# Kernel optimization log

Measured on AMD Instinct MI355X. Metric: run time of the kernel, lower is better.

## Reference

```python
import jax, jax.numpy as jnp
import numpy as np

N_QUBITS = 14
STATE_DIM = 2 ** N_QUBITS  # 16384
BATCH, SEQ = 4, 2048


def setup_inputs() -> dict:
    key = jax.random.key(0)
    ks = jax.random.split(key, 5)
    x = jax.random.normal(ks[0], (BATCH, SEQ), dtype=jnp.float32)
    rotation_params = jax.random.normal(ks[1], (N_QUBITS, 3), dtype=jnp.float32)
    entangling_params = jax.random.normal(ks[2], (N_QUBITS - 1,), dtype=jnp.float32)
    # classical_encoder: Linear(1, n_qubits) -> Tanh -> Linear(n_qubits, state_dim) -> Softmax
    W1 = jax.random.normal(ks[3], (1, N_QUBITS), dtype=jnp.float32)
    b1 = jnp.zeros((N_QUBITS,), dtype=jnp.float32)
    W2 = jax.random.normal(ks[4], (N_QUBITS, STATE_DIM), dtype=jnp.float32) * 0.1
    b2 = jnp.zeros((STATE_DIM,), dtype=jnp.float32)
    return {"x": x, "rotation_params": rotation_params,
            "entangling_params": entangling_params,
            "W1": W1, "b1": b1, "W2": W2, "b2": b2}


def reference(x, rotation_params, entangling_params, W1, b1, W2, b2):
    # classical_encoder applied to each scalar x[i,j] -> softmax weights [B,S,D]
    h = jnp.tanh(x[..., None] * W1[0] + b1)          # [B,S,nq]
    w = jax.nn.softmax(h @ W2 + b2, axis=-1)         # [B,S,D]
    # Per-qubit rotation scalar factors (independent of x), multiplied together
    half = rotation_params * 0.5
    c, s = jnp.cos(half), jnp.sin(half)              # [nq,3]
    rot_factors = c[:, 0] * c[:, 1] * c[:, 2] + 1j * (s[:, 0] * s[:, 1] * s[:, 2])
    # Per-pair parameterized-CNOT scalar factors
    cs = jax.nn.sigmoid(entangling_params)
    ent_factors = cs + 1j * (1.0 - cs)
    total = (jnp.prod(rot_factors) * jnp.prod(ent_factors)).astype(jnp.complex64)
    # state starts as e0; all scalar multiplies keep only component 0 nonzero,
    # then elementwise multiply by classical weights.
    out = jnp.zeros(w.shape, dtype=jnp.complex64)
    out = out.at[..., 0].set(total * w[..., 0].astype(jnp.complex64))
    return out
```

## Files before the change

kernel.cpp:

```cpp
#include <hip/hip_runtime.h>
#include <math.h>

constexpr int NQ    = 14;
constexpr int DIM   = 16384;
constexpr int BATCH = 4;
constexpr int SEQ   = 2048;
constexpr int NPOS  = BATCH * SEQ;
constexpr int P     = 4;
constexpr int TPB   = 256;

typedef float vf4 __attribute__((ext_vector_type(4)));
typedef float vf2 __attribute__((ext_vector_type(2)));

__device__ __forceinline__ float uniform_f(float v) {
    return __int_as_float(__builtin_amdgcn_readfirstlane(__float_as_int(v)));
}


template <bool CPLX>
__global__ void __launch_bounds__(TPB)
qenc_kernel(const float* __restrict__ x,
            const float* __restrict__ rot,
            const float* __restrict__ ent,
            const float* __restrict__ W1,
            const float* __restrict__ b1,
            const float* __restrict__ W2,
            const float* __restrict__ b2,
            float* __restrict__ out)
{
    __shared__ float sh_h[P * NQ];
    __shared__ float sh_tot_re, sh_tot_im;
    __shared__ float sh_z0[P];
    __shared__ float red[4][P];

    const int tid  = threadIdx.x;
    const int wid  = tid >> 6;
    const int lane = tid & 63;
    const long long pos0 = (long long)blockIdx.x * P;

    if (tid < P * NQ) {
        const int p = tid / NQ;
        const int k = tid - p * NQ;
        sh_h[tid] = tanhf(x[pos0 + p] * W1[k] + b1[k]);
    }
    if (tid == 64) {
        float tre = 1.0f, tim = 0.0f;
        for (int q = 0; q < NQ; ++q) {
            const float a0 = 0.5f * rot[q * 3 + 0];
            const float a1 = 0.5f * rot[q * 3 + 1];
            const float a2 = 0.5f * rot[q * 3 + 2];
            const float fre = cosf(a0) * cosf(a1) * cosf(a2);
            const float fim = sinf(a0) * sinf(a1) * sinf(a2);
            const float nre = tre * fre - tim * fim;
            const float nim = tre * fim + tim * fre;
            tre = nre; tim = nim;
        }
        for (int q = 0; q < NQ - 1; ++q) {
            const float cs  = 1.0f / (1.0f + __expf(-ent[q]));
            const float nre = tre * cs - tim * (1.0f - cs);
            const float nim = tre * (1.0f - cs) + tim * cs;
            tre = nre; tim = nim;
        }
        sh_tot_re = tre; sh_tot_im = tim;
    }
    __syncthreads();

    float h[P][NQ];
#pragma unroll
    for (int p = 0; p < P; ++p)
#pragma unroll
        for (int k = 0; k < NQ; ++k)
            h[p][k] = uniform_f(sh_h[p * NQ + k]);

    float acc[P];
#pragma unroll
    for (int p = 0; p < P; ++p) acc[p] = 0.0f;

    constexpr int ITERS = DIM / (4 * TPB);
    for (int i = 0; i < ITERS; ++i) {
        const int d = 4 * (tid + TPB * i);
        float4 wv[NQ];
#pragma unroll
        for (int k = 0; k < NQ; ++k)
            wv[k] = *reinterpret_cast<const float4*>(W2 + (size_t)k * DIM + d);
        const float4 bb = *reinterpret_cast<const float4*>(b2 + d);
        const bool d0 = (d == 0);
#pragma unroll
        for (int p = 0; p < P; ++p) {
            float za = bb.x, zb = bb.y, zc = bb.z, zd = bb.w;
#pragma unroll
            for (int k = 0; k < NQ; ++k) {
                za = fmaf(h[p][k], wv[k].x, za);
                zb = fmaf(h[p][k], wv[k].y, zb);
                zc = fmaf(h[p][k], wv[k].z, zc);
                zd = fmaf(h[p][k], wv[k].w, zd);
            }
            acc[p] += (__expf(za) + __expf(zb)) + (__expf(zc) + __expf(zd));

            if constexpr (CPLX) {
                float* rowp = out + (size_t)(pos0 + p) * (2 * (size_t)DIM) + 2 * d;
                vf4 z4 = {0.f, 0.f, 0.f, 0.f};
                if (!d0) {
                    __builtin_nontemporal_store(z4, reinterpret_cast<vf4*>(rowp));
                    __builtin_nontemporal_store(z4, reinterpret_cast<vf4*>(rowp + 4));
                } else {
                    sh_z0[p] = za;
                    vf2 z2 = {0.f, 0.f};
                    __builtin_nontemporal_store(z2, reinterpret_cast<vf2*>(rowp + 2));
                    __builtin_nontemporal_store(z4, reinterpret_cast<vf4*>(rowp + 4));
                }
            } else {
                float* rowp = out + (size_t)(pos0 + p) * (size_t)DIM + d;
                if (!d0) {
                    vf4 z4 = {0.f, 0.f, 0.f, 0.f};
                    __builtin_nontemporal_store(z4, reinterpret_cast<vf4*>(rowp));
                } else {
                    sh_z0[p] = za;
                    __builtin_nontemporal_store(0.f, rowp + 1);
                    __builtin_nontemporal_store(0.f, rowp + 2);
                    __builtin_nontemporal_store(0.f, rowp + 3);
                }
            }
        }
    }

#pragma unroll
    for (int p = 0; p < P; ++p) {
        float v = acc[p];
#pragma unroll
        for (int off = 32; off > 0; off >>= 1)
            v += __shfl_down(v, off, 64);
        if (lane == 0) red[wid][p] = v;
    }
    __syncthreads();
    if (tid < P) {
        const float denom = (red[0][tid] + red[1][tid]) + (red[2][tid] + red[3][tid]);
        const float w0 = __expf(sh_z0[tid]) / denom;
        const size_t stride = CPLX ? 2 * (size_t)DIM : (size_t)DIM;
        float* rowp = out + (size_t)(pos0 + tid) * stride;
        rowp[0] = sh_tot_re * w0;
        if constexpr (CPLX) rowp[1] = sh_tot_im * w0;
    }
}

extern "C" void kernel_launch(void* const* d_in, const int* in_sizes, int n_in,
                              void* d_out, int out_size, void* d_ws, size_t ws_size,
                              hipStream_t stream) {
    (void)in_sizes; (void)n_in; (void)d_ws; (void)ws_size;
    const float* x   = (const float*)d_in[0];
    const float* rot = (const float*)d_in[1];
    const float* ent = (const float*)d_in[2];
    const float* W1  = (const float*)d_in[3];
    const float* b1  = (const float*)d_in[4];
    const float* W2  = (const float*)d_in[5];
    const float* b2  = (const float*)d_in[6];
    float* out = (float*)d_out;

    const long long cplx_elems = (long long)NPOS * 2LL * DIM;
    if ((long long)out_size >= cplx_elems) {
        qenc_kernel<true><<<NPOS / P, TPB, 0, stream>>>(x, rot, ent, W1, b1, W2, b2, out);
    } else {
        qenc_kernel<false><<<NPOS / P, TPB, 0, stream>>>(x, rot, ent, W1, b1, W2, b2, out);
    }
}
```

Before: 567.0 us.

## Convert W2 to bf16 in workspace and process eight positions per block

Adds a pre-pass that rounds W2 to bf16 into the workspace. The main kernel then loads half-width weights and computes eight positions per block instead of four, reusing each weight load across more rows. The d==0 store branches are simplified to unconditional zero stores. This cuts W2 reload traffic and the number of blocks, but bf16 weights lower softmax accuracy, the extra h registers may hurt occupancy, and the output write (about 1 GB of complex zeros) probably still dominates.

```diff
diff --git a/kernel.cpp b/kernel.cpp
--- a/kernel.cpp
+++ b/kernel.cpp
@@ -6,7 +6,6 @@
 constexpr int BATCH = 4;
 constexpr int SEQ   = 2048;
 constexpr int NPOS  = BATCH * SEQ;
-constexpr int P     = 4;
 constexpr int TPB   = 256;
 
 typedef float vf4 __attribute__((ext_vector_type(4)));
@@ -16,18 +15,63 @@
     return __int_as_float(__builtin_amdgcn_readfirstlane(__float_as_int(v)));
 }
 
+__device__ __forceinline__ float bf16_to_f32(unsigned short u) {
+    return __uint_as_float(((unsigned int)u) << 16);
+}
+
+__global__ void __launch_bounds__(TPB)
+cvt_w2_kernel(const float* __restrict__ W2, unsigned short* __restrict__ W2b)
+{
+    const int i = (blockIdx.x * TPB + threadIdx.x) * 4;
+    const float4 v = *reinterpret_cast<const float4*>(W2 + i);
+    ushort4 r;
+    const float f[4] = {v.x, v.y, v.z, v.w};
+    unsigned short o[4];
+#pragma unroll
+    for (int j = 0; j < 4; ++j) {
+        unsigned int u = __float_as_uint(f[j]);
+        u += 0x7FFFu + ((u >> 16) & 1u);
+        o[j] = (unsigned short)(u >> 16);
+    }
+    r.x = o[0]; r.y = o[1]; r.z = o[2]; r.w = o[3];
+    *reinterpret_cast<ushort4*>(W2b + i) = r;
+}
+
+__device__ __forceinline__ void compute_total(const float* rot, const float* ent,
+                                              float* sh_tot_re, float* sh_tot_im)
+{
+    float tre = 1.0f, tim = 0.0f;
+    for (int q = 0; q < NQ; ++q) {
+        const float a0 = 0.5f * rot[q * 3 + 0];
+        const float a1 = 0.5f * rot[q * 3 + 1];
+        const float a2 = 0.5f * rot[q * 3 + 2];
+        const float fre = cosf(a0) * cosf(a1) * cosf(a2);
+        const float fim = sinf(a0) * sinf(a1) * sinf(a2);
+        const float nre = tre * fre - tim * fim;
+        const float nim = tre * fim + tim * fre;
+        tre = nre; tim = nim;
+    }
+    for (int q = 0; q < NQ - 1; ++q) {
+        const float cs  = 1.0f / (1.0f + __expf(-ent[q]));
+        const float nre = tre * cs - tim * (1.0f - cs);
+        const float nim = tre * (1.0f - cs) + tim * cs;
+        tre = nre; tim = nim;
+    }
+    *sh_tot_re = tre; *sh_tot_im = tim;
+}
 
 template <bool CPLX>
 __global__ void __launch_bounds__(TPB)
-qenc_kernel(const float* __restrict__ x,
-            const float* __restrict__ rot,
-            const float* __restrict__ ent,
-            const float* __restrict__ W1,
-            const float* __restrict__ b1,
-            const float* __restrict__ W2,
-            const float* __restrict__ b2,
-            float* __restrict__ out)
-{
+qenc_bf16_kernel(const float* __restrict__ x,
+                 const float* __restrict__ rot,
+                 const float* __restrict__ ent,
+                 const float* __restrict__ W1,
+                 const float* __restrict__ b1,
+                 const unsigned short* __restrict__ W2b,
+                 const float* __restrict__ b2,
+                 float* __restrict__ out)
+{
+    constexpr int P = 8;
     __shared__ float sh_h[P * NQ];
     __shared__ float sh_tot_re, sh_tot_im;
     __shared__ float sh_z0[P];
@@ -43,34 +87,20 @@
         const int k = tid - p * NQ;
         sh_h[tid] = tanhf(x[pos0 + p] * W1[k] + b1[k]);
     }
-    if (tid == 64) {
-        float tre = 1.0f, tim = 0.0f;
-        for (int q = 0; q < NQ; ++q) {
-            const float a0 = 0.5f * rot[q * 3 + 0];
-            const float a1 = 0.5f * rot[q * 3 + 1];
-            const float a2 = 0.5f * rot[q * 3 + 2];
-            const float fre = cosf(a0) * cosf(a1) * cosf(a2);
-            const float fim = sinf(a0) * sinf(a1) * sinf(a2);
-            const float nre = tre * fre - tim * fim;
-            const float nim = tre * fim + tim * fre;
-            tre = nre; tim = nim;
-        }
-        for (int q = 0; q < NQ - 1; ++q) {
-            const float cs  = 1.0f / (1.0f + __expf(-ent[q]));
-            const float nre = tre * cs - tim * (1.0f - cs);
-            const float nim = tre * (1.0f - cs) + tim * cs;
-            tre = nre; tim = nim;
-        }
-        sh_tot_re = tre; sh_tot_im = tim;
-    }
+    if (tid == 128) compute_total(rot, ent, &sh_tot_re, &sh_tot_im);
     __syncthreads();
 
     float h[P][NQ];
 #pragma unroll
-    for (int p = 0; p < P; ++p)
+    for (int p = 0; p < 4; ++p)
 #pragma unroll
         for (int k = 0; k < NQ; ++k)
             h[p][k] = uniform_f(sh_h[p * NQ + k]);
+#pragma unroll
+    for (int p = 4; p < P; ++p)
+#pragma unroll
+        for (int k = 0; k < NQ; ++k)
+            h[p][k] = sh_h[p * NQ + k];
 
     float acc[P];
 #pragma unroll
@@ -79,47 +109,45 @@
     constexpr int ITERS = DIM / (4 * TPB);
     for (int i = 0; i < ITERS; ++i) {
         const int d = 4 * (tid + TPB * i);
-        float4 wv[NQ];
-#pragma unroll
-        for (int k = 0; k < NQ; ++k)
-            wv[k] = *reinterpret_cast<const float4*>(W2 + (size_t)k * DIM + d);
+        ushort4 wv[NQ];
+#pragma unroll
+        for (int k = 0; k < NQ; ++k)
+            wv[k] = *reinterpret_cast<const ushort4*>(W2b + (size_t)k * DIM + d);
         const float4 bb = *reinterpret_cast<const float4*>(b2 + d);
-        const bool d0 = (d == 0);
+
+        float z[P][4];
 #pragma unroll
         for (int p = 0; p < P; ++p) {
-            float za = bb.x, zb = bb.y, zc = bb.z, zd = bb.w;
-#pragma unroll
-            for (int k = 0; k < NQ; ++k) {
-                za = fmaf(h[p][k], wv[k].x, za);
-                zb = fmaf(h[p][k], wv[k].y, zb);
-                zc = fmaf(h[p][k], wv[k].z, zc);
-                zd = fmaf(h[p][k], wv[k].w, zd);
-            }
-            acc[p] += (__expf(za) + __expf(zb)) + (__expf(zc) + __expf(zd));
-
+            z[p][0] = bb.x; z[p][1] = bb.y; z[p][2] = bb.z; z[p][3] = bb.w;
+        }
+#pragma unroll
+        for (int k = 0; k < NQ; ++k) {
+            const float c0 = bf16_to_f32(wv[k].x);
+            const float c1 = bf16_to_f32(wv[k].y);
+            const float c2 = bf16_to_f32(wv[k].z);
+            const float c3 = bf16_to_f32(wv[k].w);
+#pragma unroll
+            for (int p = 0; p < P; ++p) {
+                z[p][0] = fmaf(h[p][k], c0, z[p][0]);
+                z[p][1] = fmaf(h[p][k], c1, z[p][1]);
+                z[p][2] = fmaf(h[p][k], c2, z[p][2]);
+                z[p][3] = fmaf(h[p][k], c3, z[p][3]);
+            }
+        }
+#pragma unroll
+        for (int p = 0; p < P; ++p) {
+            acc[p] += (__expf(z[p][0]) + __expf(z[p][1]))
+                    + (__expf(z[p][2]) + __expf(z[p][3]));
+            if (d == 0) sh_z0[p] = z[p][0];
+
+            vf4 z4 = {0.f, 0.f, 0.f, 0.f};
             if constexpr (CPLX) {
                 float* rowp = out + (size_t)(pos0 + p) * (2 * (size_t)DIM) + 2 * d;
-                vf4 z4 = {0.f, 0.f, 0.f, 0.f};
-                if (!d0) {
-                    __builtin_nontemporal_store(z4, reinterpret_cast<vf4*>(rowp));
-                    __builtin_nontemporal_store(z4, reinterpret_cast<vf4*>(rowp + 4));
-                } else {
-                    sh_z0[p] = za;
-                    vf2 z2 = {0.f, 0.f};
-                    __builtin_nontemporal_store(z2, reinterpret_cast<vf2*>(rowp + 2));
-                    __builtin_nontemporal_store(z4, reinterpret_cast<vf4*>(rowp + 4));
-                }
+                __builtin_nontemporal_store(z4, reinterpret_cast<vf4*>(rowp));
+                __builtin_nontemporal_store(z4, reinterpret_cast<vf4*>(rowp + 4));
             } else {
                 float* rowp = out + (size_t)(pos0 + p) * (size_t)DIM + d;
-                if (!d0) {
-                    vf4 z4 = {0.f, 0.f, 0.f, 0.f};
-                    __builtin_nontemporal_store(z4, reinterpret_cast<vf4*>(rowp));
-                } else {
-                    sh_z0[p] = za;
-                    __builtin_nontemporal_store(0.f, rowp + 1);
-                    __builtin_nontemporal_store(0.f, rowp + 2);
-                    __builtin_nontemporal_store(0.f, rowp + 3);
-                }
+                __builtin_nontemporal_store(z4, reinterpret_cast<vf4*>(rowp));
             }
         }
     }
@@ -143,10 +171,99 @@
     }
 }
 
+template <bool CPLX>
+__global__ void __launch_bounds__(TPB)
+qenc_f32_kernel(const float* __restrict__ x, const float* __restrict__ rot,
+                const float* __restrict__ ent, const float* __restrict__ W1,
+                const float* __restrict__ b1, const float* __restrict__ W2,
+                const float* __restrict__ b2, float* __restrict__ out)
+{
+    constexpr int P = 4;
+    __shared__ float sh_h[P * NQ];
+    __shared__ float sh_tot_re, sh_tot_im;
+    __shared__ float sh_z0[P];
+    __shared__ float red[4][P];
+
+    const int tid  = threadIdx.x;
+    const int wid  = tid >> 6;
+    const int lane = tid & 63;
+    const long long pos0 = (long long)blockIdx.x * P;
+
+    if (tid < P * NQ) {
+        const int p = tid / NQ;
+        const int k = tid - p * NQ;
+        sh_h[tid] = tanhf(x[pos0 + p] * W1[k] + b1[k]);
+    }
+    if (tid == 64) compute_total(rot, ent, &sh_tot_re, &sh_tot_im);
+    __syncthreads();
+
+    float h[P][NQ];
+#pragma unroll
+    for (int p = 0; p < P; ++p)
+#pragma unroll
+        for (int k = 0; k < NQ; ++k)
+            h[p][k] = uniform_f(sh_h[p * NQ + k]);
+
+    float acc[P];
+#pragma unroll
+    for (int p = 0; p < P; ++p) acc[p] = 0.0f;
+
+    constexpr int ITERS = DIM / (4 * TPB);
+    for (int i = 0; i < ITERS; ++i) {
+        const int d = 4 * (tid + TPB * i);
+        float4 wv[NQ];
+#pragma unroll
+        for (int k = 0; k < NQ; ++k)
+            wv[k] = *reinterpret_cast<const float4*>(W2 + (size_t)k * DIM + d);
+        const float4 bb = *reinterpret_cast<const float4*>(b2 + d);
+#pragma unroll
+        for (int p = 0; p < P; ++p) {
+            float za = bb.x, zb = bb.y, zc = bb.z, zd = bb.w;
+#pragma unroll
+            for (int k = 0; k < NQ; ++k) {
+                za = fmaf(h[p][k], wv[k].x, za);
+                zb = fmaf(h[p][k], wv[k].y, zb);
+                zc = fmaf(h[p][k], wv[k].z, zc);
+                zd = fmaf(h[p][k], wv[k].w, zd);
+            }
+            acc[p] += (__expf(za) + __expf(zb)) + (__expf(zc) + __expf(zd));
+            if (d == 0) sh_z0[p] = za;
+
+            vf4 z4 = {0.f, 0.f, 0.f, 0.f};
+            if constexpr (CPLX) {
+                float* rowp = out + (size_t)(pos0 + p) * (2 * (size_t)DIM) + 2 * d;
+                __builtin_nontemporal_store(z4, reinterpret_cast<vf4*>(rowp));
+                __builtin_nontemporal_store(z4, reinterpret_cast<vf4*>(rowp + 4));
+            } else {
+                float* rowp = out + (size_t)(pos0 + p) * (size_t)DIM + d;
+                __builtin_nontemporal_store(z4, reinterpret_cast<vf4*>(rowp));
+            }
+        }
+    }
+
+#pragma unroll
+    for (int p = 0; p < P; ++p) {
+        float v = acc[p];
+#pragma unroll
+        for (int off = 32; off > 0; off >>= 1)
+            v += __shfl_down(v, off, 64);
+        if (lane == 0) red[wid][p] = v;
+    }
+    __syncthreads();
+    if (tid < P) {
+        const float denom = (red[0][tid] + red[1][tid]) + (red[2][tid] + red[3][tid]);
+        const float w0 = __expf(sh_z0[tid]) / denom;
+        const size_t stride = CPLX ? 2 * (size_t)DIM : (size_t)DIM;
+        float* rowp = out + (size_t)(pos0 + tid) * stride;
+        rowp[0] = sh_tot_re * w0;
+        if constexpr (CPLX) rowp[1] = sh_tot_im * w0;
+    }
+}
+
 extern "C" void kernel_launch(void* const* d_in, const int* in_sizes, int n_in,
                               void* d_out, int out_size, void* d_ws, size_t ws_size,
                               hipStream_t stream) {
-    (void)in_sizes; (void)n_in; (void)d_ws; (void)ws_size;
+    (void)in_sizes; (void)n_in;
     const float* x   = (const float*)d_in[0];
     const float* rot = (const float*)d_in[1];
     const float* ent = (const float*)d_in[2];
@@ -157,9 +274,20 @@
     float* out = (float*)d_out;
 
     const long long cplx_elems = (long long)NPOS * 2LL * DIM;
-    if ((long long)out_size >= cplx_elems) {
-        qenc_kernel<true><<<NPOS / P, TPB, 0, stream>>>(x, rot, ent, W1, b1, W2, b2, out);
+    const bool cplx = ((long long)out_size >= cplx_elems);
+    const size_t w2b_bytes = (size_t)NQ * DIM * sizeof(unsigned short);
+
+    if (ws_size >= w2b_bytes) {
+        unsigned short* W2b = (unsigned short*)d_ws;
+        cvt_w2_kernel<<<(NQ * DIM) / (4 * TPB), TPB, 0, stream>>>(W2, W2b);
+        if (cplx)
+            qenc_bf16_kernel<true><<<NPOS / 8, TPB, 0, stream>>>(x, rot, ent, W1, b1, W2b, b2, out);
+        else
+            qenc_bf16_kernel<false><<<NPOS / 8, TPB, 0, stream>>>(x, rot, ent, W1, b1, W2b, b2, out);
     } else {
-        qenc_kernel<false><<<NPOS / P, TPB, 0, stream>>>(x, rot, ent, W1, b1, W2, b2, out);
-    }
-}
+        if (cplx)
+            qenc_f32_kernel<true><<<NPOS / 4, TPB, 0, stream>>>(x, rot, ent, W1, b1, W2, b2, out);
+        else
+            qenc_f32_kernel<false><<<NPOS / 4, TPB, 0, stream>>>(x, rot, ent, W1, b1, W2, b2, out);
+    }
+}
```

Result: no change. 567.6 us (+0.1%).
